# Optimization experiments

Hardware: AMD Instinct MI355X
Metric: run time of the kernel (lower is better)

Reference implementation:

```python
import jax, jax.numpy as jnp
import numpy as np

B, T, I, H = 4096, 512, 3, 50


def setup_inputs() -> dict:
    key = jax.random.key(0)
    ks = jax.random.split(key, 11)
    s_i, s_h = 1.0 / np.sqrt(H), 1.0 / np.sqrt(H)
    return {
        "x": jax.random.normal(ks[0], (B, T, I), jnp.float32),
        "W_ih0": jax.random.normal(ks[1], (4 * H, I), jnp.float32) * s_i,
        "W_hh0": jax.random.normal(ks[2], (4 * H, H), jnp.float32) * s_h,
        "b_ih0": jax.random.normal(ks[3], (4 * H,), jnp.float32) * s_h,
        "b_hh0": jax.random.normal(ks[4], (4 * H,), jnp.float32) * s_h,
        "W_ih1": jax.random.normal(ks[5], (4 * H, H), jnp.float32) * s_h,
        "W_hh1": jax.random.normal(ks[6], (4 * H, H), jnp.float32) * s_h,
        "b_ih1": jax.random.normal(ks[7], (4 * H,), jnp.float32) * s_h,
        "b_hh1": jax.random.normal(ks[8], (4 * H,), jnp.float32) * s_h,
        "W_fc": jax.random.normal(ks[9], (1, H), jnp.float32) * s_h,
        "b_fc": jax.random.normal(ks[10], (1,), jnp.float32) * s_h,
    }


def _lstm_layer(x, W_ih, W_hh, b_ih, b_hh):
    # x: [B, T, D_in] -> hidden sequence [B, T, H]. PyTorch gate order i|f|g|o.
    Bt, H_ = x.shape[0], W_hh.shape[1]
    # Precompute input contribution for all timesteps (one big GEMM).
    xg = jnp.einsum('btd,gd->btg', x, W_ih) + (b_ih + b_hh)  # [B, T, 4H]

    def step(carry, xg_t):
        h, c = carry
        g = xg_t + h @ W_hh.T  # [B, 4H]
        i, f, gg, o = jnp.split(g, 4, axis=-1)
        i, f, o = jax.nn.sigmoid(i), jax.nn.sigmoid(f), jax.nn.sigmoid(o)
        c = f * c + i * jnp.tanh(gg)
        h = o * jnp.tanh(c)
        return (h, c), h

    h0 = jnp.zeros((Bt, H_), x.dtype)
    c0 = jnp.zeros((Bt, H_), x.dtype)
    (_, _), hs = jax.lax.scan(step, (h0, c0), xg.transpose(1, 0, 2))  # hs: [T, B, H]
    return hs.transpose(1, 0, 2)


def reference(x, W_ih0, W_hh0, b_ih0, b_hh0, W_ih1, W_hh1, b_ih1, b_hh1, W_fc, b_fc):
    # 2-layer LSTM, zero initial state; dropout between layers is inactive (eval mode).
    h1 = _lstm_layer(x, W_ih0, W_hh0, b_ih0, b_hh0)
    h2 = _lstm_layer(h1, W_ih1, W_hh1, b_ih1, b_hh1)
    return h2[:, -1, :] @ W_fc.T + b_fc  # [B, 1]
```

## Files before the change

### kernel.cpp

```cpp
#include <hip/hip_runtime.h>

#define SEQT 512
#define BM   16
#define NW   13
#define NT   (NW * 64)
#define ROWB 256
#define HBUF 4096

typedef _Float16 half8  __attribute__((ext_vector_type(8)));
typedef _Float16 half4v __attribute__((ext_vector_type(4)));
typedef float    f32x4  __attribute__((ext_vector_type(4)));

__device__ __forceinline__ float fast_rcp(float x) { return __builtin_amdgcn_rcpf(x); }
__device__ __forceinline__ float sigm(float x) { return fast_rcp(1.f + __expf(-x)); }
__device__ __forceinline__ float tanh_f(float x) { return 1.f - 2.f * fast_rcp(__expf(2.f * x) + 1.f); }

#define MFMA16(A, B, C) __builtin_amdgcn_mfma_f32_16x16x32_f16((A), (B), (C), 0, 0, 0)


__global__ __launch_bounds__(NT) void lstm2_mfma4(
    const float* __restrict__ x,
    const float* __restrict__ Wih0, const float* __restrict__ Whh0,
    const float* __restrict__ bih0, const float* __restrict__ bhh0,
    const float* __restrict__ Wih1, const float* __restrict__ Whh1,
    const float* __restrict__ bih1, const float* __restrict__ bhh1,
    const float* __restrict__ Wfc,  const float* __restrict__ bfc,
    float* __restrict__ out)
{
    __shared__ __align__(16) char hb[2 * HBUF];
    __shared__ float fcbuf[NW][BM];

    const int tid = threadIdx.x;
    const int l   = tid & 63, w = tid >> 6;
    const int m   = l & 15,  g4 = l >> 4;
    const int b0  = blockIdx.x * BM;
    const int swz = (m & 7) << 4;

    half8 a0h[2], a0l[2];
    half8 a1h[4], a1l[4];
    {
        const int nA = w * 16 + m;
        const int uA = nA >> 2, gA = nA & 3;
        const bool ok = uA < 50;
        const int rA = gA * 50 + (ok ? uA : 0);
#pragma unroll
        for (int kt = 0; kt < 2; ++kt) {
            half8 vh, vl;
#pragma unroll
            for (int j = 0; j < 8; ++j) {
                const int k = kt * 32 + g4 * 8 + j;
                float f = 0.f;
                if (ok) {
                    if (k < 50)                    f = Whh0[rA * 50 + k];
                    else if (k >= 52 && k < 55)    f = Wih0[rA * 3 + (k - 52)];
                    else if (k == 55)              f = bih0[rA] + bhh0[rA];
                }
                const _Float16 hi = (_Float16)f;
                vh[j] = hi; vl[j] = (_Float16)(f - (float)hi);
            }
            a0h[kt] = vh; a0l[kt] = vl;
        }
#pragma unroll
        for (int kt = 0; kt < 4; ++kt) {
            half8 vh, vl;
#pragma unroll
            for (int j = 0; j < 8; ++j) {
                const int k = kt * 32 + g4 * 8 + j;
                float f = 0.f;
                if (ok) {
                    if (k < 50)                          f = Wih1[rA * 50 + k];
                    else if (k == 55)                    f = bih1[rA] + bhh1[rA];
                    else if (k >= 64 && k < 114)         f = Whh1[rA * 50 + (k - 64)];
                }
                const _Float16 hi = (_Float16)f;
                vh[j] = hi; vl[j] = (_Float16)(f - (float)hi);
            }
            a1h[kt] = vh; a1l[kt] = vl;
        }
    }
    const int uc = w * 4 + g4;
    const float wfcv = (uc < 50) ? Wfc[uc] : 0.f;

    int rd[4];
#pragma unroll
    for (int q = 0; q < 4; ++q) rd[q] = m * ROWB + (((q * 4 + g4) * 16) ^ swz);
    const int wr0 = m * ROWB + ((uc * 2) ^ swz);
    const int wr1 = m * ROWB + (((64 + uc) * 2) ^ swz);
    const int wrx = m * ROWB + (104 ^ swz);

    for (int i = tid; i < 2 * HBUF / 4; i += NT) ((int*)hb)[i] = 0;
    __syncthreads();
    const bool xlane = (w == 0) && (g4 == 0);
    const float* xbase = x + (size_t)(b0 + m) * (SEQT * 3);
    const _Float16 onef = (_Float16)1.f;
    if (xlane) {
        half4v xv;
        xv[0] = (_Float16)xbase[0]; xv[1] = (_Float16)xbase[1];
        xv[2] = (_Float16)xbase[2]; xv[3] = onef;
        *(half4v*)(hb + HBUF + wrx) = xv;
        half4v z; z[0] = (_Float16)0.f; z[1] = z[0]; z[2] = z[0]; z[3] = onef;
        *(half4v*)(hb + wrx) = z;
    }
    float c0 = 0.f, c1 = 0.f, h1v = 0.f;
    __syncthreads();

    const f32x4 z4 = {0.f, 0.f, 0.f, 0.f};

    auto phase = [&](int rb, int wb, bool doL1, bool doX, int t) {
        const half8 bf0 = *(const half8*)(hb + rb + rd[0]);
        const half8 bf1 = *(const half8*)(hb + rb + rd[1]);
        const half8 bf2 = *(const half8*)(hb + rb + rd[2]);
        const half8 bf3 = *(const half8*)(hb + rb + rd[3]);

        f32x4 aH = MFMA16(a0h[0], bf0, z4); aH = MFMA16(a0h[1], bf1, aH);
        f32x4 aL = MFMA16(a0l[0], bf0, z4); aL = MFMA16(a0l[1], bf1, aL);

        f32x4 g1v;
        if (doL1) {
            f32x4 bH = MFMA16(a1h[0], bf0, z4); bH = MFMA16(a1h[1], bf1, bH);
            bH = MFMA16(a1h[2], bf2, bH);       bH = MFMA16(a1h[3], bf3, bH);
            f32x4 bL = MFMA16(a1l[0], bf0, z4); bL = MFMA16(a1l[1], bf1, bL);
            bL = MFMA16(a1l[2], bf2, bL);       bL = MFMA16(a1l[3], bf3, bL);
            g1v = bH + bL;
        }
        const f32x4 g0v = aH + aL;

        const float i0 = sigm(g0v[0]), f0 = sigm(g0v[1]);
        const float gg0 = tanh_f(g0v[2]), o0 = sigm(g0v[3]);
        c0 = f0 * c0 + i0 * gg0;
        const float h0 = o0 * tanh_f(c0);
        *(_Float16*)(hb + wb + wr0) = (_Float16)h0;

        if (doL1) {
            const float i1 = sigm(g1v[0]), f1 = sigm(g1v[1]);
            const float gg1 = tanh_f(g1v[2]), o1 = sigm(g1v[3]);
            c1 = f1 * c1 + i1 * gg1;
            h1v = o1 * tanh_f(c1);
            *(_Float16*)(hb + wb + wr1) = (_Float16)h1v;
        }
        if (doX && xlane) {
            const float* xp = xbase + (t + 1) * 3;
            half4v xv;
            xv[0] = (_Float16)xp[0]; xv[1] = (_Float16)xp[1];
            xv[2] = (_Float16)xp[2]; xv[3] = onef;
            *(half4v*)(hb + wb + wrx) = xv;
        }
        __syncthreads();
    };

    phase(HBUF, 0, false, true, 0);
    for (int it = 0; it < 255; ++it) {
        phase(0, HBUF, true, true, 2 * it + 1);
        phase(HBUF, 0, true, true, 2 * it + 2);
    }
    phase(0, HBUF, true, false, 511);

    {
        const half8 bf0 = *(const half8*)(hb + HBUF + rd[0]);
        const half8 bf1 = *(const half8*)(hb + HBUF + rd[1]);
        const half8 bf2 = *(const half8*)(hb + HBUF + rd[2]);
        const half8 bf3 = *(const half8*)(hb + HBUF + rd[3]);
        f32x4 bH = MFMA16(a1h[0], bf0, z4); bH = MFMA16(a1h[1], bf1, bH);
        bH = MFMA16(a1h[2], bf2, bH);       bH = MFMA16(a1h[3], bf3, bH);
        f32x4 bL = MFMA16(a1l[0], bf0, z4); bL = MFMA16(a1l[1], bf1, bL);
        bL = MFMA16(a1l[2], bf2, bL);       bL = MFMA16(a1l[3], bf3, bL);
        const f32x4 g1v = bH + bL;
        const float i1 = sigm(g1v[0]), f1 = sigm(g1v[1]);
        const float gg1 = tanh_f(g1v[2]), o1 = sigm(g1v[3]);
        c1 = f1 * c1 + i1 * gg1;
        h1v = o1 * tanh_f(c1);
    }

    float pv = h1v * wfcv;
    pv += __shfl_down(pv, 32, 64);
    pv += __shfl_down(pv, 16, 64);
    if (l < 16) fcbuf[w][l] = pv;
    __syncthreads();
    if (tid < BM) {
        float s = bfc[0];
#pragma unroll
        for (int ww = 0; ww < NW; ++ww) s += fcbuf[ww][tid];
        out[b0 + tid] = s;
    }
}

extern "C" void kernel_launch(void* const* d_in, const int* in_sizes, int n_in,
                              void* d_out, int out_size, void* d_ws, size_t ws_size,
                              hipStream_t stream)
{
    const float* x    = (const float*)d_in[0];
    const float* Wih0 = (const float*)d_in[1];
    const float* Whh0 = (const float*)d_in[2];
    const float* bih0 = (const float*)d_in[3];
    const float* bhh0 = (const float*)d_in[4];
    const float* Wih1 = (const float*)d_in[5];
    const float* Whh1 = (const float*)d_in[6];
    const float* bih1 = (const float*)d_in[7];
    const float* bhh1 = (const float*)d_in[8];
    const float* Wfc  = (const float*)d_in[9];
    const float* bfc  = (const float*)d_in[10];
    float* out = (float*)d_out;

    const int B = in_sizes[0] / (SEQT * 3);
    lstm2_mfma4<<<B / BM, NT, 0, stream>>>(x, Wih0, Whh0, bih0, bhh0,
                                           Wih1, Whh1, bih1, bhh1, Wfc, bfc, out);
}
```

Measured before the change: 566.2 us.

## Drop fp16 hi/lo split and give each wave two gate tiles

Removes the hi/lo fp16 compensation split for the weights, so each gate product uses a single MFMA pass instead of two. This halves the matrix work but lowers accuracy to plain fp16 weights. Each wavefront now covers two 16-row gate tiles, which cuts the block from 13 waves to 7 and reduces the cost of the per-step block barrier. The layer-1 accumulation is split into two independent chains to shorten MFMA dependency latency.

```diff
diff --git a/kernel.cpp b/kernel.cpp
--- a/kernel.cpp
+++ b/kernel.cpp
@@ -2,7 +2,7 @@
 
 #define SEQT 512
 #define BM   16
-#define NW   13
+#define NW   7
 #define NT   (NW * 64)
 #define ROWB 256
 #define HBUF 4096
@@ -18,7 +18,7 @@
 #define MFMA16(A, B, C) __builtin_amdgcn_mfma_f32_16x16x32_f16((A), (B), (C), 0, 0, 0)
 
 
-__global__ __launch_bounds__(NT) void lstm2_mfma4(
+__global__ __launch_bounds__(NT) void lstm2_mfma5(
     const float* __restrict__ x,
     const float* __restrict__ Wih0, const float* __restrict__ Whh0,
     const float* __restrict__ bih0, const float* __restrict__ bhh0,
@@ -35,57 +35,66 @@
     const int m   = l & 15,  g4 = l >> 4;
     const int b0  = blockIdx.x * BM;
     const int swz = (m & 7) << 4;
-
-    half8 a0h[2], a0l[2];
-    half8 a1h[4], a1l[4];
-    {
-        const int nA = w * 16 + m;
+    const bool hasT1 = (w < 6);
+
+    half8 a0[2][2];
+    half8 a1[2][4];
+    float wfcv[2];
+    int   ucv[2];
+    bool  wok[2];
+#pragma unroll
+    for (int tt = 0; tt < 2; ++tt) {
+        const int T  = 2 * w + tt;
+        const int nA = T * 16 + m;
         const int uA = nA >> 2, gA = nA & 3;
         const bool ok = uA < 50;
         const int rA = gA * 50 + (ok ? uA : 0);
 #pragma unroll
         for (int kt = 0; kt < 2; ++kt) {
-            half8 vh, vl;
+            half8 v;
 #pragma unroll
             for (int j = 0; j < 8; ++j) {
                 const int k = kt * 32 + g4 * 8 + j;
                 float f = 0.f;
                 if (ok) {
-                    if (k < 50)                    f = Whh0[rA * 50 + k];
-                    else if (k >= 52 && k < 55)    f = Wih0[rA * 3 + (k - 52)];
-                    else if (k == 55)              f = bih0[rA] + bhh0[rA];
+                    if (k < 50)                 f = Whh0[rA * 50 + k];
+                    else if (k >= 52 && k < 55) f = Wih0[rA * 3 + (k - 52)];
+                    else if (k == 55)           f = bih0[rA] + bhh0[rA];
                 }
-                const _Float16 hi = (_Float16)f;
-                vh[j] = hi; vl[j] = (_Float16)(f - (float)hi);
-            }
-            a0h[kt] = vh; a0l[kt] = vl;
+                v[j] = (_Float16)f;
+            }
+            a0[tt][kt] = v;
         }
 #pragma unroll
         for (int kt = 0; kt < 4; ++kt) {
-            half8 vh, vl;
+            half8 v;
 #pragma unroll
             for (int j = 0; j < 8; ++j) {
                 const int k = kt * 32 + g4 * 8 + j;
                 float f = 0.f;
                 if (ok) {
-                    if (k < 50)                          f = Wih1[rA * 50 + k];
-                    else if (k == 55)                    f = bih1[rA] + bhh1[rA];
-                    else if (k >= 64 && k < 114)         f = Whh1[rA * 50 + (k - 64)];
+                    if (k < 50)                  f = Wih1[rA * 50 + k];
+                    else if (k == 55)            f = bih1[rA] + bhh1[rA];
+                    else if (k >= 64 && k < 114) f = Whh1[rA * 50 + (k - 64)];
                 }
-                const _Float16 hi = (_Float16)f;
-                vh[j] = hi; vl[j] = (_Float16)(f - (float)hi);
-            }
-            a1h[kt] = vh; a1l[kt] = vl;
-        }
-    }
-    const int uc = w * 4 + g4;
-    const float wfcv = (uc < 50) ? Wfc[uc] : 0.f;
-
-    int rd[4];
+                v[j] = (_Float16)f;
+            }
+            a1[tt][kt] = v;
+        }
+        const int uc = T * 4 + g4;
+        ucv[tt]  = uc;
+        wok[tt]  = (uc < 50);
+        wfcv[tt] = (uc < 50) ? Wfc[uc] : 0.f;
+    }
+
+    int rd[4], wr0[2], wr1[2];
 #pragma unroll
     for (int q = 0; q < 4; ++q) rd[q] = m * ROWB + (((q * 4 + g4) * 16) ^ swz);
-    const int wr0 = m * ROWB + ((uc * 2) ^ swz);
-    const int wr1 = m * ROWB + (((64 + uc) * 2) ^ swz);
+#pragma unroll
+    for (int tt = 0; tt < 2; ++tt) {
+        wr0[tt] = m * ROWB + ((ucv[tt] * 2) ^ swz);
+        wr1[tt] = m * ROWB + (((64 + ucv[tt]) * 2) ^ swz);
+    }
     const int wrx = m * ROWB + (104 ^ swz);
 
     for (int i = tid; i < 2 * HBUF / 4; i += NT) ((int*)hb)[i] = 0;
@@ -101,7 +110,7 @@
         half4v z; z[0] = (_Float16)0.f; z[1] = z[0]; z[2] = z[0]; z[3] = onef;
         *(half4v*)(hb + wrx) = z;
     }
-    float c0 = 0.f, c1 = 0.f, h1v = 0.f;
+    float c0[2] = {0.f, 0.f}, c1[2] = {0.f, 0.f}, h1v[2] = {0.f, 0.f};
     __syncthreads();
 
     const f32x4 z4 = {0.f, 0.f, 0.f, 0.f};
@@ -112,31 +121,37 @@
         const half8 bf2 = *(const half8*)(hb + rb + rd[2]);
         const half8 bf3 = *(const half8*)(hb + rb + rd[3]);
 
-        f32x4 aH = MFMA16(a0h[0], bf0, z4); aH = MFMA16(a0h[1], bf1, aH);
-        f32x4 aL = MFMA16(a0l[0], bf0, z4); aL = MFMA16(a0l[1], bf1, aL);
-
-        f32x4 g1v;
+        f32x4 gA0, gA1, gB0, gB1;
+        gA0 = MFMA16(a0[0][0], bf0, z4); gA0 = MFMA16(a0[0][1], bf1, gA0);
+        if (hasT1) { gA1 = MFMA16(a0[1][0], bf0, z4); gA1 = MFMA16(a0[1][1], bf1, gA1); }
         if (doL1) {
-            f32x4 bH = MFMA16(a1h[0], bf0, z4); bH = MFMA16(a1h[1], bf1, bH);
-            bH = MFMA16(a1h[2], bf2, bH);       bH = MFMA16(a1h[3], bf3, bH);
-            f32x4 bL = MFMA16(a1l[0], bf0, z4); bL = MFMA16(a1l[1], bf1, bL);
-            bL = MFMA16(a1l[2], bf2, bL);       bL = MFMA16(a1l[3], bf3, bL);
-            g1v = bH + bL;
-        }
-        const f32x4 g0v = aH + aL;
-
-        const float i0 = sigm(g0v[0]), f0 = sigm(g0v[1]);
-        const float gg0 = tanh_f(g0v[2]), o0 = sigm(g0v[3]);
-        c0 = f0 * c0 + i0 * gg0;
-        const float h0 = o0 * tanh_f(c0);
-        *(_Float16*)(hb + wb + wr0) = (_Float16)h0;
-
-        if (doL1) {
-            const float i1 = sigm(g1v[0]), f1 = sigm(g1v[1]);
-            const float gg1 = tanh_f(g1v[2]), o1 = sigm(g1v[3]);
-            c1 = f1 * c1 + i1 * gg1;
-            h1v = o1 * tanh_f(c1);
-            *(_Float16*)(hb + wb + wr1) = (_Float16)h1v;
+            f32x4 p = MFMA16(a1[0][0], bf0, z4); p = MFMA16(a1[0][1], bf1, p);
+            f32x4 q = MFMA16(a1[0][2], bf2, z4); q = MFMA16(a1[0][3], bf3, q);
+            gB0 = p + q;
+            if (hasT1) {
+                f32x4 r = MFMA16(a1[1][0], bf0, z4); r = MFMA16(a1[1][1], bf1, r);
+                f32x4 s = MFMA16(a1[1][2], bf2, z4); s = MFMA16(a1[1][3], bf3, s);
+                gB1 = r + s;
+            }
+        }
+
+#pragma unroll
+        for (int tt = 0; tt < 2; ++tt) {
+            if (tt == 1 && !hasT1) break;
+            const f32x4 g0v = (tt == 0) ? gA0 : gA1;
+            const float i0 = sigm(g0v[0]), f0 = sigm(g0v[1]);
+            const float gg0 = tanh_f(g0v[2]), o0 = sigm(g0v[3]);
+            c0[tt] = f0 * c0[tt] + i0 * gg0;
+            const float h0 = o0 * tanh_f(c0[tt]);
+            if (wok[tt]) *(_Float16*)(hb + wb + wr0[tt]) = (_Float16)h0;
+            if (doL1) {
+                const f32x4 g1v = (tt == 0) ? gB0 : gB1;
+                const float i1 = sigm(g1v[0]), f1 = sigm(g1v[1]);
+                const float gg1 = tanh_f(g1v[2]), o1 = sigm(g1v[3]);
+                c1[tt] = f1 * c1[tt] + i1 * gg1;
+                h1v[tt] = o1 * tanh_f(c1[tt]);
+                if (wok[tt]) *(_Float16*)(hb + wb + wr1[tt]) = (_Float16)h1v[tt];
+            }
         }
         if (doX && xlane) {
             const float* xp = xbase + (t + 1) * 3;
@@ -160,18 +175,20 @@
         const half8 bf1 = *(const half8*)(hb + HBUF + rd[1]);
         const half8 bf2 = *(const half8*)(hb + HBUF + rd[2]);
         const half8 bf3 = *(const half8*)(hb + HBUF + rd[3]);
-        f32x4 bH = MFMA16(a1h[0], bf0, z4); bH = MFMA16(a1h[1], bf1, bH);
-        bH = MFMA16(a1h[2], bf2, bH);       bH = MFMA16(a1h[3], bf3, bH);
-        f32x4 bL = MFMA16(a1l[0], bf0, z4); bL = MFMA16(a1l[1], bf1, bL);
-        bL = MFMA16(a1l[2], bf2, bL);       bL = MFMA16(a1l[3], bf3, bL);
-        const f32x4 g1v = bH + bL;
-        const float i1 = sigm(g1v[0]), f1 = sigm(g1v[1]);
-        const float gg1 = tanh_f(g1v[2]), o1 = sigm(g1v[3]);
-        c1 = f1 * c1 + i1 * gg1;
-        h1v = o1 * tanh_f(c1);
-    }
-
-    float pv = h1v * wfcv;
+#pragma unroll
+        for (int tt = 0; tt < 2; ++tt) {
+            if (tt == 1 && !hasT1) break;
+            f32x4 p = MFMA16(a1[tt][0], bf0, z4); p = MFMA16(a1[tt][1], bf1, p);
+            f32x4 q = MFMA16(a1[tt][2], bf2, z4); q = MFMA16(a1[tt][3], bf3, q);
+            const f32x4 g1v = p + q;
+            const float i1 = sigm(g1v[0]), f1 = sigm(g1v[1]);
+            const float gg1 = tanh_f(g1v[2]), o1 = sigm(g1v[3]);
+            c1[tt] = f1 * c1[tt] + i1 * gg1;
+            h1v[tt] = o1 * tanh_f(c1[tt]);
+        }
+    }
+
+    float pv = h1v[0] * wfcv[0] + h1v[1] * wfcv[1];
     pv += __shfl_down(pv, 32, 64);
     pv += __shfl_down(pv, 16, 64);
     if (l < 16) fcbuf[w][l] = pv;
@@ -202,6 +219,6 @@
     float* out = (float*)d_out;
 
     const int B = in_sizes[0] / (SEQT * 3);
-    lstm2_mfma4<<<B / BM, NT, 0, stream>>>(x, Wih0, Whh0, bih0, bhh0,
+    lstm2_mfma5<<<B / BM, NT, 0, stream>>>(x, Wih0, Whh0, bih0, bhh0,
                                            Wih1, Whh1, bih1, bhh1, Wfc, bfc, out);
 }
```

New measurement: 540.1 us. 1.05x faster.
